# Kernel tuning notes

Measured on AMD Instinct MI355X. Metric: run time of the kernel, lower is better.

Reference implementation:

```python
import jax, jax.numpy as jnp
import numpy as np

C = 256  # channels (depthwise: groups == out_channels == in_channels)


def _dwconv(x, w, b):
    # x: [B,C,H,W], w: [C,1,3,3] (OIHW), b: [C]; depthwise 3x3, padding=1
    out = jax.lax.conv_general_dilated(
        x, w,
        window_strides=(1, 1),
        padding=((1, 1), (1, 1)),
        dimension_numbers=('NCHW', 'OIHW', 'NCHW'),
        feature_group_count=C,
    )
    return out + b[None, :, None, None]


def setup_inputs() -> dict:
    key = jax.random.key(0)
    k1, k2, k3, k4 = jax.random.split(key, 4)
    B, H, W = 8, 128, 128
    x = jax.random.normal(k1, (B, C, H, W), dtype=jnp.float32)
    y = jax.random.normal(k2, (B, C, H, W), dtype=jnp.float32)
    # torch Conv2d default init: U(-sqrt(k), sqrt(k)), k = 1/(fan_in) = 1/(1*3*3)
    bound = 1.0 / np.sqrt(9.0)
    conv_w = jax.random.uniform(k3, (C, 1, 3, 3), dtype=jnp.float32, minval=-bound, maxval=bound)
    conv_b = jax.random.uniform(k4, (C,), dtype=jnp.float32, minval=-bound, maxval=bound)
    return {"x": x, "y": y, "conv_w": conv_w, "conv_b": conv_b}


def reference(x, y, conv_w, conv_b):
    # Forget gate
    f_feat = _dwconv(y, conv_w, conv_b)
    f_gate = jax.nn.sigmoid(f_feat)
    # Update gate
    u_gate = f_gate * jnp.tanh(f_feat)
    # Stage and output (same conv weights applied again)
    x_stage = x * f_gate + u_gate
    output_y = jnp.tanh(_dwconv(x_stage, conv_w, conv_b)) * f_gate + y + y
    return output_y
```

## Files before the change

kernel.cpp:

```cpp
#include <hip/hip_runtime.h>
#include <math.h>

#define HW   128
#define BH   8
#define C_CH 256

__device__ __forceinline__ void sig_tanh(float s, float& fg, float& th) {
    float sc = fminf(15.f, fmaxf(-15.f, s));
    float t  = __expf(-sc);
    fg = __builtin_amdgcn_rcpf(1.f + t);
    float t2 = t * t;
    th = (1.f - t2) * __builtin_amdgcn_rcpf(1.f + t2);
}

__device__ __forceinline__ float tanh_fast(float s) {
    float sc = fminf(15.f, fmaxf(-15.f, s));
    float t2 = __expf(-2.f * sc);
    return (1.f - t2) * __builtin_amdgcn_rcpf(1.f + t2);
}

__device__ __forceinline__ void row_acc(float w0, float w1, float w2,
    float l, const float4& a, const float4& b, float r,
    float4& s0, float4& s1)
{
    s0.x = fmaf(w0, l,   fmaf(w1, a.x, fmaf(w2, a.y, s0.x)));
    s0.y = fmaf(w0, a.x, fmaf(w1, a.y, fmaf(w2, a.z, s0.y)));
    s0.z = fmaf(w0, a.y, fmaf(w1, a.z, fmaf(w2, a.w, s0.z)));
    s0.w = fmaf(w0, a.z, fmaf(w1, a.w, fmaf(w2, b.x, s0.w)));
    s1.x = fmaf(w0, a.w, fmaf(w1, b.x, fmaf(w2, b.y, s1.x)));
    s1.y = fmaf(w0, b.x, fmaf(w1, b.y, fmaf(w2, b.z, s1.y)));
    s1.z = fmaf(w0, b.y, fmaf(w1, b.z, fmaf(w2, b.w, s1.z)));
    s1.w = fmaf(w0, b.z, fmaf(w1, b.w, fmaf(w2, r,   s1.w)));
}

__global__ __launch_bounds__(256, 4) void fused_gated_dwconv_reg(
    const float* __restrict__ x, const float* __restrict__ y,
    const float* __restrict__ w, const float* __restrict__ b,
    float* __restrict__ out)
{
    const int tid   = threadIdx.x;
    const int s     = tid & 15;
    const int band  = tid >> 4;
    const int plane = blockIdx.x;
    const int c     = plane & (C_CH - 1);
    const int rb    = band * BH;
    const int col0  = s * 8;

    const size_t poff = (size_t)plane * (HW * HW);
    const float* yp = y + poff + col0;
    const float* xp = x + poff + col0;
    float*       op = out + poff + col0;

    float wk[9];
    #pragma unroll
    for (int k = 0; k < 9; ++k) wk[k] = w[c * 9 + k];
    const float bias = b[c];

    float  yl[3], yr[3];  float4 ya[3], yb[3];
    float  xl[3], xr[3];  float4 xa[3], xb[3];
    float4 fa[2], fb[2];

    #pragma unroll
    for (int t = 0; t < BH + 4; ++t) {
        {
            int gy = rb - 2 + t;
            bool iny = (unsigned)gy < (unsigned)HW;
            const float* p = yp + (size_t)(iny ? gy : 0) * HW;
            float4 a  = *reinterpret_cast<const float4*>(p);
            float4 bb = *reinterpret_cast<const float4*>(p + 4);
            if (!iny) { a = make_float4(0.f,0.f,0.f,0.f); bb = make_float4(0.f,0.f,0.f,0.f); }
            float l = __shfl_up(bb.w, 1, 16);  if (s == 0)  l = 0.f;
            float r = __shfl_down(a.x, 1, 16); if (s == 15) r = 0.f;
            const int sl = t % 3;
            yl[sl] = l; ya[sl] = a; yb[sl] = bb; yr[sl] = r;
        }
        if (t >= 2) {
            int qx = rb - 3 + t;
            bool inx = (unsigned)qx < (unsigned)HW;
            const float* p = xp + (size_t)(inx ? qx : 0) * HW;
            float4 xva = *reinterpret_cast<const float4*>(p);
            float4 xvb = *reinterpret_cast<const float4*>(p + 4);

            const int i0 = (t - 2) % 3, i1 = (t - 1) % 3, i2 = t % 3;
            float4 s0 = make_float4(bias, bias, bias, bias), s1 = s0;
            row_acc(wk[0], wk[1], wk[2], yl[i0], ya[i0], yb[i0], yr[i0], s0, s1);
            row_acc(wk[3], wk[4], wk[5], yl[i1], ya[i1], yb[i1], yr[i1], s0, s1);
            row_acc(wk[6], wk[7], wk[8], yl[i2], ya[i2], yb[i2], yr[i2], s0, s1);

            float4 fga, fgb, tha, thb;
            sig_tanh(s0.x, fga.x, tha.x);
            sig_tanh(s0.y, fga.y, tha.y);
            sig_tanh(s0.z, fga.z, tha.z);
            sig_tanh(s0.w, fga.w, tha.w);
            sig_tanh(s1.x, fgb.x, thb.x);
            sig_tanh(s1.y, fgb.y, thb.y);
            sig_tanh(s1.z, fgb.z, thb.z);
            sig_tanh(s1.w, fgb.w, thb.w);

            float4 xsa, xsb;
            xsa.x = fga.x * (xva.x + tha.x);
            xsa.y = fga.y * (xva.y + tha.y);
            xsa.z = fga.z * (xva.z + tha.z);
            xsa.w = fga.w * (xva.w + tha.w);
            xsb.x = fgb.x * (xvb.x + thb.x);
            xsb.y = fgb.y * (xvb.y + thb.y);
            xsb.z = fgb.z * (xvb.z + thb.z);
            xsb.w = fgb.w * (xvb.w + thb.w);
            if (!inx) { xsa = make_float4(0.f,0.f,0.f,0.f); xsb = make_float4(0.f,0.f,0.f,0.f); }

            float l = __shfl_up(xsb.w, 1, 16);  if (s == 0)  l = 0.f;
            float r = __shfl_down(xsa.x, 1, 16); if (s == 15) r = 0.f;
            xl[i2] = l; xa[i2] = xsa; xb[i2] = xsb; xr[i2] = r;
            fa[t & 1] = fga; fb[t & 1] = fgb;
        }
        if (t >= 4) {
            int r = rb - 4 + t;
            const int i0 = (t - 2) % 3, i1 = (t - 1) % 3, i2 = t % 3;
            float4 s0 = make_float4(bias, bias, bias, bias), s1 = s0;
            row_acc(wk[0], wk[1], wk[2], xl[i0], xa[i0], xb[i0], xr[i0], s0, s1);
            row_acc(wk[3], wk[4], wk[5], xl[i1], xa[i1], xb[i1], xr[i1], s0, s1);
            row_acc(wk[6], wk[7], wk[8], xl[i2], xa[i2], xb[i2], xr[i2], s0, s1);

            const float4 fga = fa[(t + 1) & 1];
            const float4 fgb = fb[(t + 1) & 1];
            const int iy = (t - 2) % 3;

            float4 o0, o1;
            o0.x = fmaf(tanh_fast(s0.x), fga.x, 2.f * ya[iy].x);
            o0.y = fmaf(tanh_fast(s0.y), fga.y, 2.f * ya[iy].y);
            o0.z = fmaf(tanh_fast(s0.z), fga.z, 2.f * ya[iy].z);
            o0.w = fmaf(tanh_fast(s0.w), fga.w, 2.f * ya[iy].w);
            o1.x = fmaf(tanh_fast(s1.x), fgb.x, 2.f * yb[iy].x);
            o1.y = fmaf(tanh_fast(s1.y), fgb.y, 2.f * yb[iy].y);
            o1.z = fmaf(tanh_fast(s1.z), fgb.z, 2.f * yb[iy].z);
            o1.w = fmaf(tanh_fast(s1.w), fgb.w, 2.f * yb[iy].w);

            float* po = op + (size_t)r * HW;
            *reinterpret_cast<float4*>(po)     = o0;
            *reinterpret_cast<float4*>(po + 4) = o1;
        }
    }
}

extern "C" void kernel_launch(void* const* d_in, const int* in_sizes, int n_in,
                              void* d_out, int out_size, void* d_ws, size_t ws_size,
                              hipStream_t stream) {
    const float* x = (const float*)d_in[0];
    const float* y = (const float*)d_in[1];
    const float* w = (const float*)d_in[2];
    const float* b = (const float*)d_in[3];
    float* out = (float*)d_out;

    const int planes = in_sizes[0] / (HW * HW);
    dim3 grid(planes);
    dim3 block(256);
    fused_gated_dwconv_reg<<<grid, block, 0, stream>>>(x, y, w, b, out);
}
```

Before: 99.92 us.

## Replace lane shuffles with redundant halo loads and recompute gated halo columns

Cross-lane shuffles for the column halos are removed. Each thread now loads a 2-column halo of y and a 1-column halo of x straight from memory, then recomputes the first conv, sigmoid and tanh for the two edge columns itself. That adds 25% more first-conv FMAs and transcendentals per row, plus extra small global loads, in exchange for removing shuffle latency and the dependency between lanes. The tanh formulas are also rewritten as 2/(1+e)-1 to save one multiply.

New measurement: 100.0 us. About the same (+0.1%).

```diff
diff --git a/kernel.cpp b/kernel.cpp
--- a/kernel.cpp
+++ b/kernel.cpp
@@ -5,35 +5,50 @@
 #define BH   8
 #define C_CH 256
 
+struct R12 { float l0, l1; float4 a, b; float r0, r1; };
+struct R10 { float l;      float4 a, b; float r;      };
+
 __device__ __forceinline__ void sig_tanh(float s, float& fg, float& th) {
     float sc = fminf(15.f, fmaxf(-15.f, s));
     float t  = __expf(-sc);
+    float t2 = t * t;
     fg = __builtin_amdgcn_rcpf(1.f + t);
-    float t2 = t * t;
-    th = (1.f - t2) * __builtin_amdgcn_rcpf(1.f + t2);
+    th = fmaf(2.f, __builtin_amdgcn_rcpf(1.f + t2), -1.f);
 }
 
 __device__ __forceinline__ float tanh_fast(float s) {
     float sc = fminf(15.f, fmaxf(-15.f, s));
     float t2 = __expf(-2.f * sc);
-    return (1.f - t2) * __builtin_amdgcn_rcpf(1.f + t2);
+    return fmaf(2.f, __builtin_amdgcn_rcpf(1.f + t2), -1.f);
 }
 
-__device__ __forceinline__ void row_acc(float w0, float w1, float w2,
-    float l, const float4& a, const float4& b, float r,
-    float4& s0, float4& s1)
-{
-    s0.x = fmaf(w0, l,   fmaf(w1, a.x, fmaf(w2, a.y, s0.x)));
-    s0.y = fmaf(w0, a.x, fmaf(w1, a.y, fmaf(w2, a.z, s0.y)));
-    s0.z = fmaf(w0, a.y, fmaf(w1, a.z, fmaf(w2, a.w, s0.z)));
-    s0.w = fmaf(w0, a.z, fmaf(w1, a.w, fmaf(w2, b.x, s0.w)));
-    s1.x = fmaf(w0, a.w, fmaf(w1, b.x, fmaf(w2, b.y, s1.x)));
-    s1.y = fmaf(w0, b.x, fmaf(w1, b.y, fmaf(w2, b.z, s1.y)));
-    s1.z = fmaf(w0, b.y, fmaf(w1, b.z, fmaf(w2, b.w, s1.z)));
-    s1.w = fmaf(w0, b.z, fmaf(w1, b.w, fmaf(w2, r,   s1.w)));
+__device__ __forceinline__ void facc(float w0, float w1, float w2,
+                                     const R12& y, R10& s) {
+    s.l   = fmaf(w0, y.l0,  fmaf(w1, y.l1,  fmaf(w2, y.a.x, s.l)));
+    s.a.x = fmaf(w0, y.l1,  fmaf(w1, y.a.x, fmaf(w2, y.a.y, s.a.x)));
+    s.a.y = fmaf(w0, y.a.x, fmaf(w1, y.a.y, fmaf(w2, y.a.z, s.a.y)));
+    s.a.z = fmaf(w0, y.a.y, fmaf(w1, y.a.z, fmaf(w2, y.a.w, s.a.z)));
+    s.a.w = fmaf(w0, y.a.z, fmaf(w1, y.a.w, fmaf(w2, y.b.x, s.a.w)));
+    s.b.x = fmaf(w0, y.a.w, fmaf(w1, y.b.x, fmaf(w2, y.b.y, s.b.x)));
+    s.b.y = fmaf(w0, y.b.x, fmaf(w1, y.b.y, fmaf(w2, y.b.z, s.b.y)));
+    s.b.z = fmaf(w0, y.b.y, fmaf(w1, y.b.z, fmaf(w2, y.b.w, s.b.z)));
+    s.b.w = fmaf(w0, y.b.z, fmaf(w1, y.b.w, fmaf(w2, y.r0,  s.b.w)));
+    s.r   = fmaf(w0, y.b.w, fmaf(w1, y.r0,  fmaf(w2, y.r1,  s.r)));
 }
 
-__global__ __launch_bounds__(256, 4) void fused_gated_dwconv_reg(
+__device__ __forceinline__ void oacc(float w0, float w1, float w2,
+                                     const R10& v, float4& s0, float4& s1) {
+    s0.x = fmaf(w0, v.l,   fmaf(w1, v.a.x, fmaf(w2, v.a.y, s0.x)));
+    s0.y = fmaf(w0, v.a.x, fmaf(w1, v.a.y, fmaf(w2, v.a.z, s0.y)));
+    s0.z = fmaf(w0, v.a.y, fmaf(w1, v.a.z, fmaf(w2, v.a.w, s0.z)));
+    s0.w = fmaf(w0, v.a.z, fmaf(w1, v.a.w, fmaf(w2, v.b.x, s0.w)));
+    s1.x = fmaf(w0, v.a.w, fmaf(w1, v.b.x, fmaf(w2, v.b.y, s1.x)));
+    s1.y = fmaf(w0, v.b.x, fmaf(w1, v.b.y, fmaf(w2, v.b.z, s1.y)));
+    s1.z = fmaf(w0, v.b.y, fmaf(w1, v.b.z, fmaf(w2, v.b.w, s1.z)));
+    s1.w = fmaf(w0, v.b.z, fmaf(w1, v.b.w, fmaf(w2, v.r,   s1.w)));
+}
+
+__global__ __launch_bounds__(256, 4) void fused_gated_dwconv_nh(
     const float* __restrict__ x, const float* __restrict__ y,
     const float* __restrict__ w, const float* __restrict__ b,
     float* __restrict__ out)
@@ -45,20 +60,21 @@
     const int c     = plane & (C_CH - 1);
     const int rb    = band * BH;
     const int col0  = s * 8;
+    const bool sL = (s == 0), sR = (s == 15);
 
     const size_t poff = (size_t)plane * (HW * HW);
-    const float* yp = y + poff + col0;
-    const float* xp = x + poff + col0;
-    float*       op = out + poff + col0;
+    const float* yp = y + poff;
+    const float* xp = x + poff;
+    float*       op = out + poff;
 
     float wk[9];
     #pragma unroll
     for (int k = 0; k < 9; ++k) wk[k] = w[c * 9 + k];
     const float bias = b[c];
 
-    float  yl[3], yr[3];  float4 ya[3], yb[3];
-    float  xl[3], xr[3];  float4 xa[3], xb[3];
-    float4 fa[2], fb[2];
+    R12 yw[3];
+    R10 xw[3];
+    float4 fga[2], fgb[2];
 
     #pragma unroll
     for (int t = 0; t < BH + 4; ++t) {
@@ -66,76 +82,88 @@
             int gy = rb - 2 + t;
             bool iny = (unsigned)gy < (unsigned)HW;
             const float* p = yp + (size_t)(iny ? gy : 0) * HW;
-            float4 a  = *reinterpret_cast<const float4*>(p);
-            float4 bb = *reinterpret_cast<const float4*>(p + 4);
-            if (!iny) { a = make_float4(0.f,0.f,0.f,0.f); bb = make_float4(0.f,0.f,0.f,0.f); }
-            float l = __shfl_up(bb.w, 1, 16);  if (s == 0)  l = 0.f;
-            float r = __shfl_down(a.x, 1, 16); if (s == 15) r = 0.f;
-            const int sl = t % 3;
-            yl[sl] = l; ya[sl] = a; yb[sl] = bb; yr[sl] = r;
+            float2 lv = *reinterpret_cast<const float2*>(p + (sL ? col0 : col0 - 2));
+            float4 av = *reinterpret_cast<const float4*>(p + col0);
+            float4 bv = *reinterpret_cast<const float4*>(p + col0 + 4);
+            float2 rv = *reinterpret_cast<const float2*>(p + (sR ? col0 : col0 + 8));
+            R12 Y;
+            bool okL = iny && !sL, okR = iny && !sR;
+            Y.l0 = okL ? lv.x : 0.f;
+            Y.l1 = okL ? lv.y : 0.f;
+            Y.a  = iny ? av : make_float4(0.f, 0.f, 0.f, 0.f);
+            Y.b  = iny ? bv : make_float4(0.f, 0.f, 0.f, 0.f);
+            Y.r0 = okR ? rv.x : 0.f;
+            Y.r1 = okR ? rv.y : 0.f;
+            yw[t % 3] = Y;
         }
         if (t >= 2) {
-            int qx = rb - 3 + t;
-            bool inx = (unsigned)qx < (unsigned)HW;
-            const float* p = xp + (size_t)(inx ? qx : 0) * HW;
-            float4 xva = *reinterpret_cast<const float4*>(p);
-            float4 xvb = *reinterpret_cast<const float4*>(p + 4);
+            int q = rb - 3 + t;
+            bool inx = (unsigned)q < (unsigned)HW;
+            const float* p = xp + (size_t)(inx ? q : 0) * HW;
+            float  xl = *(p + (sL ? col0 : col0 - 1));
+            float4 xa = *reinterpret_cast<const float4*>(p + col0);
+            float4 xb = *reinterpret_cast<const float4*>(p + col0 + 4);
+            float  xr = *(p + (sR ? col0 : col0 + 8));
 
-            const int i0 = (t - 2) % 3, i1 = (t - 1) % 3, i2 = t % 3;
-            float4 s0 = make_float4(bias, bias, bias, bias), s1 = s0;
-            row_acc(wk[0], wk[1], wk[2], yl[i0], ya[i0], yb[i0], yr[i0], s0, s1);
-            row_acc(wk[3], wk[4], wk[5], yl[i1], ya[i1], yb[i1], yr[i1], s0, s1);
-            row_acc(wk[6], wk[7], wk[8], yl[i2], ya[i2], yb[i2], yr[i2], s0, s1);
+            R10 F;
+            F.l = bias; F.a = make_float4(bias, bias, bias, bias); F.b = F.a; F.r = bias;
+            facc(wk[0], wk[1], wk[2], yw[(t - 2) % 3], F);
+            facc(wk[3], wk[4], wk[5], yw[(t - 1) % 3], F);
+            facc(wk[6], wk[7], wk[8], yw[t % 3],       F);
 
-            float4 fga, fgb, tha, thb;
-            sig_tanh(s0.x, fga.x, tha.x);
-            sig_tanh(s0.y, fga.y, tha.y);
-            sig_tanh(s0.z, fga.z, tha.z);
-            sig_tanh(s0.w, fga.w, tha.w);
-            sig_tanh(s1.x, fgb.x, thb.x);
-            sig_tanh(s1.y, fgb.y, thb.y);
-            sig_tanh(s1.z, fgb.z, thb.z);
-            sig_tanh(s1.w, fgb.w, thb.w);
+            float fgl, thl, fgr, thr;
+            float4 fa, ta, fb, tb;
+            sig_tanh(F.l,   fgl,  thl);
+            sig_tanh(F.a.x, fa.x, ta.x);
+            sig_tanh(F.a.y, fa.y, ta.y);
+            sig_tanh(F.a.z, fa.z, ta.z);
+            sig_tanh(F.a.w, fa.w, ta.w);
+            sig_tanh(F.b.x, fb.x, tb.x);
+            sig_tanh(F.b.y, fb.y, tb.y);
+            sig_tanh(F.b.z, fb.z, tb.z);
+            sig_tanh(F.b.w, fb.w, tb.w);
+            sig_tanh(F.r,   fgr,  thr);
 
-            float4 xsa, xsb;
-            xsa.x = fga.x * (xva.x + tha.x);
-            xsa.y = fga.y * (xva.y + tha.y);
-            xsa.z = fga.z * (xva.z + tha.z);
-            xsa.w = fga.w * (xva.w + tha.w);
-            xsb.x = fgb.x * (xvb.x + thb.x);
-            xsb.y = fgb.y * (xvb.y + thb.y);
-            xsb.z = fgb.z * (xvb.z + thb.z);
-            xsb.w = fgb.w * (xvb.w + thb.w);
-            if (!inx) { xsa = make_float4(0.f,0.f,0.f,0.f); xsb = make_float4(0.f,0.f,0.f,0.f); }
-
-            float l = __shfl_up(xsb.w, 1, 16);  if (s == 0)  l = 0.f;
-            float r = __shfl_down(xsa.x, 1, 16); if (s == 15) r = 0.f;
-            xl[i2] = l; xa[i2] = xsa; xb[i2] = xsb; xr[i2] = r;
-            fa[t & 1] = fga; fb[t & 1] = fgb;
+            R10 XS;
+            XS.l   = (inx && !sL) ? fgl * (xl + thl) : 0.f;
+            XS.a.x = fa.x * (xa.x + ta.x);
+            XS.a.y = fa.y * (xa.y + ta.y);
+            XS.a.z = fa.z * (xa.z + ta.z);
+            XS.a.w = fa.w * (xa.w + ta.w);
+            XS.b.x = fb.x * (xb.x + tb.x);
+            XS.b.y = fb.y * (xb.y + tb.y);
+            XS.b.z = fb.z * (xb.z + tb.z);
+            XS.b.w = fb.w * (xb.w + tb.w);
+            XS.r   = (inx && !sR) ? fgr * (xr + thr) : 0.f;
+            if (!inx) {
+                XS.a = make_float4(0.f, 0.f, 0.f, 0.f);
+                XS.b = make_float4(0.f, 0.f, 0.f, 0.f);
+            }
+            xw[t % 3] = XS;
+            fga[t & 1] = fa; fgb[t & 1] = fb;
         }
         if (t >= 4) {
             int r = rb - 4 + t;
-            const int i0 = (t - 2) % 3, i1 = (t - 1) % 3, i2 = t % 3;
             float4 s0 = make_float4(bias, bias, bias, bias), s1 = s0;
-            row_acc(wk[0], wk[1], wk[2], xl[i0], xa[i0], xb[i0], xr[i0], s0, s1);
-            row_acc(wk[3], wk[4], wk[5], xl[i1], xa[i1], xb[i1], xr[i1], s0, s1);
-            row_acc(wk[6], wk[7], wk[8], xl[i2], xa[i2], xb[i2], xr[i2], s0, s1);
+            oacc(wk[0], wk[1], wk[2], xw[(t - 2) % 3], s0, s1);
+            oacc(wk[3], wk[4], wk[5], xw[(t - 1) % 3], s0, s1);
+            oacc(wk[6], wk[7], wk[8], xw[t % 3],       s0, s1);
 
-            const float4 fga = fa[(t + 1) & 1];
-            const float4 fgb = fb[(t + 1) & 1];
-            const int iy = (t - 2) % 3;
+            const float4 fa = fga[(t + 1) & 1];
+            const float4 fb = fgb[(t + 1) & 1];
+            const R12&  Y  = yw[(t - 2) % 3];
 
             float4 o0, o1;
-            o0.x = fmaf(tanh_fast(s0.x), fga.x, 2.f * ya[iy].x);
-            o0.y = fmaf(tanh_fast(s0.y), fga.y, 2.f * ya[iy].y);
-            o0.z = fmaf(tanh_fast(s0.z), fga.z, 2.f * ya[iy].z);
-            o0.w = fmaf(tanh_fast(s0.w), fga.w, 2.f * ya[iy].w);
-            o1.x = fmaf(tanh_fast(s1.x), fgb.x, 2.f * yb[iy].x);
-            o1.y = fmaf(tanh_fast(s1.y), fgb.y, 2.f * yb[iy].y);
-            o1.z = fmaf(tanh_fast(s1.z), fgb.z, 2.f * yb[iy].z);
-            o1.w = fmaf(tanh_fast(s1.w), fgb.w, 2.f * yb[iy].w);
+            o0.x = fmaf(tanh_fast(s0.x), fa.x, 2.f * Y.a.x);
+            o0.y = fmaf(tanh_fast(s0.y), fa.y, 2.f * Y.a.y);
+            o0.z = fmaf(tanh_fast(s0.z), fa.z, 2.f * Y.a.z);
+            o0.w = fmaf(tanh_fast(s0.w), fa.w, 2.f * Y.a.w);
+            o1.x = fmaf(tanh_fast(s1.x), fb.x, 2.f * Y.b.x);
+            o1.y = fmaf(tanh_fast(s1.y), fb.y, 2.f * Y.b.y);
+            o1.z = fmaf(tanh_fast(s1.z), fb.z, 2.f * Y.b.z);
+            o1.w = fmaf(tanh_fast(s1.w), fb.w, 2.f * Y.b.w);
 
-            float* po = op + (size_t)r * HW;
+            float* po = op + (size_t)r * HW + col0;
             *reinterpret_cast<float4*>(po)     = o0;
             *reinterpret_cast<float4*>(po + 4) = o1;
         }
@@ -154,5 +182,5 @@
     const int planes = in_sizes[0] / (HW * HW);
     dim3 grid(planes);
     dim3 block(256);
-    fused_gated_dwconv_reg<<<grid, block, 0, stream>>>(x, y, w, b, out);
+    fused_gated_dwconv_nh<<<grid, block, 0, stream>>>(x, y, w, b, out);
 }
```
